# Kernel tuning notes

Measured on AMD Instinct MI355X. Metric: run time of the kernel, lower is better.

The kernel has to match this reference:

```python
import jax, jax.numpy as jnp
import numpy as np

M, T, D = 4, 8192, 64   # d = d_qk + 2 = 64; last channel is time
NLIN = 3                # n_layers=2 hidden linears + output linear


def setup_inputs() -> dict:
    key = jax.random.key(0)
    ks = jax.random.split(key, 7)
    X = jax.random.normal(ks[0], (M, T, D), dtype=jnp.float32)
    # last feature channel is a sorted timestamp per modality
    times = jnp.sort(jax.random.uniform(ks[1], (M, T), dtype=jnp.float32) * 100.0, axis=1)
    X = X.at[:, :, -1].set(times)
    s = 1.0 / np.sqrt(D).astype(np.float32)
    wq_w = jax.random.normal(ks[2], (NLIN, D, D), dtype=jnp.float32) * s
    wq_b = jax.random.normal(ks[3], (NLIN, D), dtype=jnp.float32) * 0.01
    wk_w = jax.random.normal(ks[4], (M, NLIN, D, D), dtype=jnp.float32) * s
    wk_b = jax.random.normal(ks[5], (M, NLIN, D), dtype=jnp.float32) * 0.01
    return {"X": X, "wq_w": wq_w, "wq_b": wq_b, "wk_w": wk_w, "wk_b": wk_b}


def mlp(x, W, b):
    # W: (NLIN, D, D), b: (NLIN, D); relu on all but the last linear
    for i in range(NLIN - 1):
        x = jax.nn.relu(x @ W[i] + b[i])
    return x @ W[-1] + b[-1]


def causal_dot_product(Q, K, V, t1, t2):
    # out[i] = Q[i] @ sum_{j: t2[j] <= t1[i]} K[j] (outer) V[j]
    S = jnp.cumsum(K[:, :, None] * V[:, None, :], axis=0)  # (T, D, D) prefix K^T V state
    idx = jnp.searchsorted(t2, t1, side="right") - 1       # last key with t2 <= t1[i]
    Sg = jnp.where((idx >= 0)[:, None, None], S[jnp.clip(idx, 0, T - 1)], 0.0)
    return jnp.einsum("td,tde->te", Q, Sg)                   # (T, D)


def reference(X, wq_w, wq_b, wk_w, wk_b):
    t1 = X[0, :, -1]               # query times from modality m1
    Q = mlp(X[0], wq_w, wq_b)      # (T, D)

    def per_modality(Xm, Wm, bm):
        K = mlp(Xm, Wm, bm)        # (T, D)
        V = Xm                     # V = X in original
        t2 = Xm[:, -1]
        return causal_dot_product(Q, K, V, t1, t2)

    Z = jax.vmap(per_modality)(X, wk_w, wk_b)  # (M, T, D) == Zout[0]
    yhat = Z.sum(0)[:, :2]                     # Zout.sum(1)[..., :2]
    return yhat[None]                          # (1, T, 2)
```

## Files before the change

kernel.cpp:

```cpp
#include <hip/hip_runtime.h>

#define TT 8192
#define DD 64
#define MODS 4
#define NCH 256
#define CH  32

typedef __attribute__((ext_vector_type(8))) short bf16x8;
typedef __attribute__((ext_vector_type(4))) float f32x4;

__device__ __forceinline__ unsigned f2bf1(float x) {
    unsigned u = __float_as_uint(x);
    return (u + 0x7FFFu + ((u >> 16) & 1u)) >> 16;
}
__device__ __forceinline__ unsigned packbf(float a, float b) {
    return f2bf1(a) | (f2bf1(b) << 16);
}

__device__ __forceinline__ void stage_w(const float* __restrict__ Wl,
                                        unsigned short* wb, int c, int dp0)
{
    #pragma unroll
    for (int it = 0; it < 8; ++it) {
        int dp = dp0 + 4 * it;
        float w0 = Wl[(2 * dp)     * DD + c];
        float w1 = Wl[(2 * dp + 1) * DD + c];
        *(unsigned*)&wb[c * 72 + 2 * dp] = packbf(w0, w1);
    }
}

__global__ __launch_bounds__(256)
void mlp_scan(const float* __restrict__ X,
              const float* __restrict__ wq_w, const float* __restrict__ wq_b,
              const float* __restrict__ wk_w, const float* __restrict__ wk_b,
              float* __restrict__ Q, float* __restrict__ Kout,
              float* __restrict__ Ctot, float* __restrict__ Csub,
              float* __restrict__ times)
{
    __shared__ unsigned short xbuf[4][16][72];
    __shared__ unsigned short wbuf[2][64][72];
    __shared__ float kbuf[64][68];
    __shared__ float2 vstash[64];

    const int job = blockIdx.y;
    const float *xin, *Wj, *Bias;
    float* out;
    if (job == 0) { xin = X; Wj = wq_w; Bias = wq_b; out = Q; }
    else {
        const int m = job - 1;
        xin  = X    + (size_t)m * TT * DD;
        Wj   = wk_w + (size_t)m * 3 * DD * DD;
        Bias = wk_b + (size_t)m * 3 * DD;
        out  = Kout + (size_t)m * TT * DD;
    }

    const int t    = threadIdx.x;
    const int wv   = t >> 6;
    const int lane = t & 63;
    const int quad = lane >> 4;
    const int l15  = lane & 15;
    const int row0 = blockIdx.x * 64 + wv * 16;
    unsigned short* xb = &xbuf[wv][0][0];
    const int wc = t & 63, wdp0 = t >> 6;

    {
        const float4* src = (const float4*)(xin + (size_t)row0 * DD);
        #pragma unroll
        for (int k = 0; k < 4; ++k) {
            int f = lane + 64 * k;
            int r = f >> 4, c4 = (f & 15) << 2;
            float4 v = src[f];
            if (job > 0) {
                if ((f & 15) == 0)  vstash[wv * 16 + r] = make_float2(v.x, v.y);
                if ((f & 15) == 15) times[(size_t)(job - 1) * TT + row0 + r] = v.w;
            }
            uint2 p = make_uint2(packbf(v.x, v.y), packbf(v.z, v.w));
            *(uint2*)&xb[r * 72 + c4] = p;
        }
    }

    stage_w(Wj, &wbuf[0][0][0], wc, wdp0);

    #pragma unroll
    for (int l = 0; l < 3; ++l) {
        __syncthreads();
        const unsigned short* wb = &wbuf[l & 1][0][0];
        if (l < 2)
            stage_w(Wj + (size_t)(l + 1) * DD * DD, &wbuf[(l + 1) & 1][0][0], wc, wdp0);

        const float* Bl = Bias + l * DD;
        f32x4 acc[4];
        #pragma unroll
        for (int mt = 0; mt < 4; ++mt) {
            float4 b4 = *(const float4*)(Bl + 16 * mt + quad * 4);
            acc[mt][0] = b4.x; acc[mt][1] = b4.y; acc[mt][2] = b4.z; acc[mt][3] = b4.w;
        }

        bf16x8 xf[2];
        #pragma unroll
        for (int kt = 0; kt < 2; ++kt)
            xf[kt] = *(const bf16x8*)&xb[l15 * 72 + quad * 8 + kt * 32];

        #pragma unroll
        for (int mt = 0; mt < 4; ++mt) {
            #pragma unroll
            for (int kt = 0; kt < 2; ++kt) {
                bf16x8 wf = *(const bf16x8*)&wb[(16 * mt + l15) * 72 + quad * 8 + kt * 32];
                acc[mt] = __builtin_amdgcn_mfma_f32_16x16x32_bf16(wf, xf[kt], acc[mt], 0, 0, 0);
            }
        }

        if (l < 2) {
            #pragma unroll
            for (int mt = 0; mt < 4; ++mt) {
                float r0 = fmaxf(acc[mt][0], 0.f), r1 = fmaxf(acc[mt][1], 0.f);
                float r2 = fmaxf(acc[mt][2], 0.f), r3 = fmaxf(acc[mt][3], 0.f);
                uint2 p = make_uint2(packbf(r0, r1), packbf(r2, r3));
                *(uint2*)&xb[l15 * 72 + 16 * mt + quad * 4] = p;
            }
        } else {
            #pragma unroll
            for (int mt = 0; mt < 4; ++mt) {
                float4 v = make_float4(acc[mt][0], acc[mt][1], acc[mt][2], acc[mt][3]);
                *(float4*)(out + (size_t)(row0 + l15) * DD + 16 * mt + quad * 4) = v;
                if (job > 0)
                    *(float4*)(&kbuf[wv * 16 + l15][16 * mt + quad * 4]) = v;
            }
        }
    }

    if (job > 0) {
        __syncthreads();
        const int m    = job - 1;
        const int chl  = t >> 7;
        const int tid2 = t & 127;
        const int d = tid2 & 63, e = tid2 >> 6;
        const int ch = blockIdx.x * 2 + chl;
        float acc = 0.f;
        #pragma unroll
        for (int j = 0; j < 4; ++j) {
            #pragma unroll
            for (int s = 0; s < 8; ++s) {
                const int rr = chl * 32 + j * 8 + s;
                float kv = kbuf[rr][d];
                float vv = e ? vstash[rr].y : vstash[rr].x;
                acc = fmaf(kv, vv, acc);
            }
            if (j < 3)
                Csub[(((size_t)m * NCH + ch) * 3 + j) * 128 + tid2] = acc;
        }
        Ctot[((size_t)m * NCH + ch) * 128 + tid2] = acc;
    }
}

__global__ __launch_bounds__(256)
void prefix_find(const float* __restrict__ Ctot, float* __restrict__ PreC,
                 const float* __restrict__ times, int* __restrict__ idx)
{
    const int b = blockIdx.x;
    if (b < MODS) {
        __shared__ float hs[128];
        const int sub = threadIdx.x >> 7, t = threadIdx.x & 127;
        const size_t base = ((size_t)b * NCH + (size_t)sub * 128) * 128 + t;

        float tot = 0.f;
        #pragma unroll 8
        for (int c = 0; c < 128; ++c)
            tot += Ctot[base + (size_t)c * 128];
        if (sub == 0) hs[t] = tot;
        __syncthreads();

        float run = sub ? hs[t] : 0.f;
        #pragma unroll 1
        for (int bb = 0; bb < 16; ++bb) {
            float v[8];
            #pragma unroll
            for (int i = 0; i < 8; ++i)
                v[i] = Ctot[base + (size_t)(bb * 8 + i) * 128];
            #pragma unroll
            for (int i = 0; i < 8; ++i) {
                PreC[base + (size_t)(bb * 8 + i) * 128] = run;
                run += v[i];
            }
        }
    } else {
        const int bb = b - MODS;
        const int m  = bb >> 5;
        const int q  = ((bb & 31) << 8) + threadIdx.x;
        const float t1 = times[q];
        const float* t2 = times + (size_t)m * TT;
        int lo = 0, hi = TT;
        #pragma unroll 1
        for (int s = 0; s < 13; ++s) {
            int mid = (lo + hi) >> 1;
            bool le = (t2[mid] <= t1);
            lo = le ? mid + 1 : lo;
            hi = le ? hi : mid;
        }
        idx[(size_t)m * TT + q] = lo - 1;
    }
}

__global__ __launch_bounds__(256)
void gather_kernel(const float* __restrict__ X, const float* __restrict__ Q,
                   const float* __restrict__ Kin, const float* __restrict__ Csub,
                   const float* __restrict__ PreC, const int* __restrict__ idx,
                   float* __restrict__ out)
{
    const int bx   = blockIdx.x;
    const int q    = ((bx & 7) << 10) | (bx >> 3);
    const int m    = threadIdx.x >> 6;
    const int lane = threadIdx.x & 63;

    const float qv = Q[(size_t)q * DD + lane];
    const int id = idx[(size_t)m * TT + q];

    float a0 = 0.f, a1 = 0.f;
    if (id >= 0) {
        const int cg = id >> 5;
        const float* P = PreC + ((size_t)(m * NCH + cg) << 7);
        float s0 = P[lane], s1 = P[64 + lane];
        const int n = id - cg * CH;
        const int j = n >> 3;
        if (j > 0) {
            const float* Sr = Csub + (((size_t)m * NCH + cg) * 3 + (j - 1)) * 128;
            s0 += Sr[lane]; s1 += Sr[64 + lane];
        }
        const float* Kb = Kin + ((size_t)m * TT + (size_t)cg * CH) * DD;
        const float* Vb = X   + ((size_t)m * TT + (size_t)cg * CH) * DD;
        #pragma unroll 1
        for (int tt = j * 8; tt <= n; ++tt) {
            float kv = Kb[tt * DD + lane];
            float2 vv = *(const float2*)(Vb + tt * DD);
            s0 = fmaf(kv, vv.x, s0);
            s1 = fmaf(kv, vv.y, s1);
        }
        a0 = qv * s0;
        a1 = qv * s1;
    }
    #pragma unroll
    for (int off = 32; off > 0; off >>= 1) {
        a0 += __shfl_xor(a0, off, 64);
        a1 += __shfl_xor(a1, off, 64);
    }
    __shared__ float red[MODS][2];
    if (lane == 0) { red[m][0] = a0; red[m][1] = a1; }
    __syncthreads();
    if (threadIdx.x == 0) {
        out[(q << 1)]     = red[0][0] + red[1][0] + red[2][0] + red[3][0];
        out[(q << 1) + 1] = red[0][1] + red[1][1] + red[2][1] + red[3][1];
    }
}

extern "C" void kernel_launch(void* const* d_in, const int* in_sizes, int n_in,
                              void* d_out, int out_size, void* d_ws, size_t ws_size,
                              hipStream_t stream)
{
    const float* X    = (const float*)d_in[0];
    const float* wq_w = (const float*)d_in[1];
    const float* wq_b = (const float*)d_in[2];
    const float* wk_w = (const float*)d_in[3];
    const float* wk_b = (const float*)d_in[4];
    float* out = (float*)d_out;

    float* ws    = (float*)d_ws;
    float* Q     = ws;
    float* K     = Q     + (size_t)TT * DD;
    float* Ctot  = K     + (size_t)MODS * TT * DD;
    float* PreC  = Ctot  + (size_t)MODS * NCH * 128;
    float* Csub  = PreC  + (size_t)MODS * NCH * 128;
    float* times = Csub  + (size_t)MODS * NCH * 3 * 128;
    int*   idx   = (int*)(times + (size_t)MODS * TT);

    mlp_scan     <<<dim3(128, 5),  256, 0, stream>>>(X, wq_w, wq_b, wk_w, wk_b,
                                                     Q, K, Ctot, Csub, times);
    prefix_find  <<<MODS + 128,    256, 0, stream>>>(Ctot, PreC, times, idx);
    gather_kernel<<<TT,            256, 0, stream>>>(X, Q, K, Csub, PreC, idx, out);
}
```

Before: 99.28 us.

## Store per-row intra-chunk prefix states and gather without serial tail loop

The MLP/scan kernel now writes the full within-chunk running K^T V prefix (128 floats per row) to a new Crow buffer instead of K and sub-chunk partial sums. The gather kernel then forms each state as chunk prefix plus row prefix, with no serial loop over up to 8 K/V rows. It also handles 8 queries per block to cut the block count. The trade-off is far more global writes (4×8192×128 floats) in exchange for a constant-time gather.

```diff
diff --git a/kernel.cpp b/kernel.cpp
--- a/kernel.cpp
+++ b/kernel.cpp
@@ -5,6 +5,7 @@
 #define MODS 4
 #define NCH 256
 #define CH  32
+#define QPB 8
 
 typedef __attribute__((ext_vector_type(8))) short bf16x8;
 typedef __attribute__((ext_vector_type(4))) float f32x4;
@@ -33,9 +34,8 @@
 void mlp_scan(const float* __restrict__ X,
               const float* __restrict__ wq_w, const float* __restrict__ wq_b,
               const float* __restrict__ wk_w, const float* __restrict__ wk_b,
-              float* __restrict__ Q, float* __restrict__ Kout,
-              float* __restrict__ Ctot, float* __restrict__ Csub,
-              float* __restrict__ times)
+              float* __restrict__ Q, float* __restrict__ Ctot,
+              float* __restrict__ Crow, float* __restrict__ times)
 {
     __shared__ unsigned short xbuf[4][16][72];
     __shared__ unsigned short wbuf[2][64][72];
@@ -44,14 +44,12 @@
 
     const int job = blockIdx.y;
     const float *xin, *Wj, *Bias;
-    float* out;
-    if (job == 0) { xin = X; Wj = wq_w; Bias = wq_b; out = Q; }
+    if (job == 0) { xin = X; Wj = wq_w; Bias = wq_b; }
     else {
         const int m = job - 1;
         xin  = X    + (size_t)m * TT * DD;
         Wj   = wk_w + (size_t)m * 3 * DD * DD;
         Bias = wk_b + (size_t)m * 3 * DD;
-        out  = Kout + (size_t)m * TT * DD;
     }
 
     const int t    = threadIdx.x;
@@ -122,8 +120,9 @@
             #pragma unroll
             for (int mt = 0; mt < 4; ++mt) {
                 float4 v = make_float4(acc[mt][0], acc[mt][1], acc[mt][2], acc[mt][3]);
-                *(float4*)(out + (size_t)(row0 + l15) * DD + 16 * mt + quad * 4) = v;
-                if (job > 0)
+                if (job == 0)
+                    *(float4*)(Q + (size_t)(row0 + l15) * DD + 16 * mt + quad * 4) = v;
+                else
                     *(float4*)(&kbuf[wv * 16 + l15][16 * mt + quad * 4]) = v;
             }
         }
@@ -136,18 +135,19 @@
         const int tid2 = t & 127;
         const int d = tid2 & 63, e = tid2 >> 6;
         const int ch = blockIdx.x * 2 + chl;
+        const size_t rbase = ((size_t)m * TT + (size_t)ch * CH) * 128 + tid2;
         float acc = 0.f;
         #pragma unroll
         for (int j = 0; j < 4; ++j) {
             #pragma unroll
             for (int s = 0; s < 8; ++s) {
-                const int rr = chl * 32 + j * 8 + s;
+                const int r  = j * 8 + s;
+                const int rr = chl * 32 + r;
                 float kv = kbuf[rr][d];
                 float vv = e ? vstash[rr].y : vstash[rr].x;
                 acc = fmaf(kv, vv, acc);
-            }
-            if (j < 3)
-                Csub[(((size_t)m * NCH + ch) * 3 + j) * 128 + tid2] = acc;
+                Crow[rbase + (size_t)r * 128] = acc;
+            }
         }
         Ctot[((size_t)m * NCH + ch) * 128 + tid2] = acc;
     }
@@ -202,53 +202,46 @@
 }
 
 __global__ __launch_bounds__(256)
-void gather_kernel(const float* __restrict__ X, const float* __restrict__ Q,
-                   const float* __restrict__ Kin, const float* __restrict__ Csub,
+void gather_kernel(const float* __restrict__ Q,
+                   const float* __restrict__ Crow,
                    const float* __restrict__ PreC, const int* __restrict__ idx,
                    float* __restrict__ out)
 {
     const int bx   = blockIdx.x;
-    const int q    = ((bx & 7) << 10) | (bx >> 3);
+    const int q0   = ((bx & 7) << 10) | ((bx >> 3) << 3);
     const int m    = threadIdx.x >> 6;
     const int lane = threadIdx.x & 63;
 
-    const float qv = Q[(size_t)q * DD + lane];
-    const int id = idx[(size_t)m * TT + q];
-
-    float a0 = 0.f, a1 = 0.f;
-    if (id >= 0) {
-        const int cg = id >> 5;
-        const float* P = PreC + ((size_t)(m * NCH + cg) << 7);
-        float s0 = P[lane], s1 = P[64 + lane];
-        const int n = id - cg * CH;
-        const int j = n >> 3;
-        if (j > 0) {
-            const float* Sr = Csub + (((size_t)m * NCH + cg) * 3 + (j - 1)) * 128;
-            s0 += Sr[lane]; s1 += Sr[64 + lane];
-        }
-        const float* Kb = Kin + ((size_t)m * TT + (size_t)cg * CH) * DD;
-        const float* Vb = X   + ((size_t)m * TT + (size_t)cg * CH) * DD;
-        #pragma unroll 1
-        for (int tt = j * 8; tt <= n; ++tt) {
-            float kv = Kb[tt * DD + lane];
-            float2 vv = *(const float2*)(Vb + tt * DD);
-            s0 = fmaf(kv, vv.x, s0);
-            s1 = fmaf(kv, vv.y, s1);
-        }
-        a0 = qv * s0;
-        a1 = qv * s1;
-    }
+    __shared__ float red[QPB][MODS][2];
+
+    const int* idxm = idx + (size_t)m * TT;
     #pragma unroll
-    for (int off = 32; off > 0; off >>= 1) {
-        a0 += __shfl_xor(a0, off, 64);
-        a1 += __shfl_xor(a1, off, 64);
-    }
-    __shared__ float red[MODS][2];
-    if (lane == 0) { red[m][0] = a0; red[m][1] = a1; }
+    for (int u = 0; u < QPB; ++u) {
+        const int q  = q0 + u;
+        const int id = idxm[q];
+        float a0 = 0.f, a1 = 0.f;
+        if (id >= 0) {
+            const float qv = Q[(size_t)q * DD + lane];
+            const int cg = id >> 5;
+            const float* P = PreC + ((size_t)(m * NCH + cg) << 7);
+            const float* R = Crow + (((size_t)m * TT + id) << 7);
+            float s0 = P[lane]      + R[lane];
+            float s1 = P[64 + lane] + R[64 + lane];
+            a0 = qv * s0;
+            a1 = qv * s1;
+        }
+        #pragma unroll
+        for (int off = 32; off > 0; off >>= 1) {
+            a0 += __shfl_xor(a0, off, 64);
+            a1 += __shfl_xor(a1, off, 64);
+        }
+        if (lane == 0) { red[u][m][0] = a0; red[u][m][1] = a1; }
+    }
     __syncthreads();
-    if (threadIdx.x == 0) {
-        out[(q << 1)]     = red[0][0] + red[1][0] + red[2][0] + red[3][0];
-        out[(q << 1) + 1] = red[0][1] + red[1][1] + red[2][1] + red[3][1];
+    if (threadIdx.x < QPB * 2) {
+        const int u = threadIdx.x >> 1, e = threadIdx.x & 1;
+        out[((q0 + u) << 1) + e] =
+            red[u][0][e] + red[u][1][e] + red[u][2][e] + red[u][3][e];
     }
 }
 
@@ -265,15 +258,14 @@
 
     float* ws    = (float*)d_ws;
     float* Q     = ws;
-    float* K     = Q     + (size_t)TT * DD;
-    float* Ctot  = K     + (size_t)MODS * TT * DD;
+    float* Crow  = Q     + (size_t)TT * DD;
+    float* Ctot  = Crow  + (size_t)MODS * TT * 128;
     float* PreC  = Ctot  + (size_t)MODS * NCH * 128;
-    float* Csub  = PreC  + (size_t)MODS * NCH * 128;
-    float* times = Csub  + (size_t)MODS * NCH * 3 * 128;
+    float* times = PreC  + (size_t)MODS * NCH * 128;
     int*   idx   = (int*)(times + (size_t)MODS * TT);
 
     mlp_scan     <<<dim3(128, 5),  256, 0, stream>>>(X, wq_w, wq_b, wk_w, wk_b,
-                                                     Q, K, Ctot, Csub, times);
+                                                     Q, Ctot, Crow, times);
     prefix_find  <<<MODS + 128,    256, 0, stream>>>(Ctot, PreC, times, idx);
-    gather_kernel<<<TT,            256, 0, stream>>>(X, Q, K, Csub, PreC, idx, out);
-}
+    gather_kernel<<<TT / QPB,      256, 0, stream>>>(Q, Crow, PreC, idx, out);
+}
```

Result: faster. 91.76 us (-7.6%).
